# Kernel optimization log

Measured on AMD Instinct MI355X. Metric: run time of the kernel, lower is better.

The kernel has to match this reference:

```python
import jax, jax.numpy as jnp
import numpy as np

N = 50000      # nodes
E = 800000     # edges (avg degree 16)
IN = 128       # in_features
H = 4          # num_heads
OUT = 32       # out_features per head
NEG_SLOPE = 0.2


def setup_inputs() -> dict:
    key = jax.random.key(0)
    k1, k2, k3, k4 = jax.random.split(key, 4)
    h = jax.random.normal(k1, (N, IN), dtype=jnp.float32)
    edge_index = jax.random.randint(k2, (2, E), 0, N, dtype=jnp.int32)
    # xavier-ish init scales
    W = jax.random.normal(k3, (H, IN, OUT), dtype=jnp.float32) * np.float32(np.sqrt(2.0 / (IN + OUT)))
    a = jax.random.normal(k4, (H, 2 * OUT), dtype=jnp.float32) * np.float32(np.sqrt(2.0 / (2 * OUT)))
    return {"h": h, "edge_index": edge_index, "W": W, "a": a}


def reference(h, edge_index, W, a):
    src, dst = edge_index[0], edge_index[1]
    # project per head: [N, H, OUT]
    h_proj = jnp.einsum('ni,hio->nho', h, W)
    # score = leaky_relu(a . [Wh_src || Wh_dst]) ; split a to avoid materializing the concat
    a_src, a_dst = a[:, :OUT], a[:, OUT:]
    s_src = jnp.einsum('nho,ho->nh', h_proj, a_src)   # [N, H]
    s_dst = jnp.einsum('nho,ho->nh', h_proj, a_dst)   # [N, H]
    score = jax.nn.leaky_relu(s_src[src] + s_dst[dst], negative_slope=NEG_SLOPE)  # [E, H]
    # sparse softmax over incoming edges of each dst node
    smax = jax.ops.segment_max(score, dst, num_segments=N)          # [N, H]
    smax = jnp.where(jnp.isfinite(smax), smax, jnp.float32(-1e9))   # nodes with no in-edges
    score_exp = jnp.exp(score - smax[dst])                          # [E, H]
    denom = jax.ops.segment_sum(score_exp, dst, num_segments=N)     # [N, H]
    denom = jnp.maximum(denom, jnp.float32(1e-16))
    alpha = score_exp / denom[dst]                                  # [E, H]
    # weighted aggregation (dropout is identity in eval mode)
    h_src = h_proj[src]                                             # [E, H, OUT]
    h_out = jax.ops.segment_sum(alpha[:, :, None] * h_src, dst, num_segments=N)  # [N, H, OUT]
    h_out = h_out.reshape(N, H * OUT)  # concat=True
    return jax.nn.elu(h_out)
```

## Files before the change

kernel.cpp:

```cpp
#include <hip/hip_runtime.h>

#define NEG_SLOPE 0.2f
#define BCAP 8192

typedef __attribute__((ext_vector_type(8))) short short8;
typedef __attribute__((ext_vector_type(4))) float floatx4;

__device__ __forceinline__ unsigned f2bf(float x) {
  unsigned u = __float_as_uint(x);
  unsigned r = ((u >> 16) & 1u) + 0x7fffu;
  return (u + r) >> 16;
}
__device__ __forceinline__ float bf2f(unsigned hi16) {
  return __uint_as_float(hi16 << 16);
}

__global__ __launch_bounds__(256) void k_gemm(const float* __restrict__ h,
                                              const float* __restrict__ W,
                                              const float* __restrict__ a,
                                              const int* __restrict__ ei,
                                              int* __restrict__ bcur,
                                              uint2* __restrict__ gpairs,
                                              unsigned short* __restrict__ hp16,
                                              float* __restrict__ ssrc,
                                              float* __restrict__ sdst,
                                              int N, int E, int NB1, int NB2) {
  __shared__ unsigned lds_u[16384];
  const int tid = threadIdx.x;

  if (blockIdx.x < NB1) {
    uint2* stage = (uint2*)lds_u;
    int* cnt = (int*)&lds_u[8192];
    int* start = (int*)&lds_u[8448];
    int* cur = (int*)&lds_u[8704];
    int* gbase = (int*)&lds_u[8960];
    int* scn = (int*)&lds_u[9216];
    const int e0 = blockIdx.x * 4096;
    for (int i = tid; i < NB2; i += 256) cnt[i] = 0;
    __syncthreads();
    int sarr[16], darr[16];
#pragma unroll
    for (int j = 0; j < 16; ++j) {
      int e = e0 + j * 256 + tid;
      if (e < E) {
        sarr[j] = ei[e];
        darr[j] = ei[E + e];
        atomicAdd(&cnt[darr[j] >> 8], 1);
      } else {
        darr[j] = -1;
      }
    }
    __syncthreads();
    int s = (tid < NB2) ? cnt[tid] : 0;
    scn[tid] = s;
    __syncthreads();
    for (int off = 1; off < 256; off <<= 1) {
      int t = (tid >= off) ? scn[tid - off] : 0;
      __syncthreads();
      scn[tid] += t;
      __syncthreads();
    }
    if (tid < NB2) {
      start[tid] = scn[tid] - s;
      cur[tid] = scn[tid] - s;
      gbase[tid] = s ? atomicAdd(&bcur[tid], s) : 0;
    }
    __syncthreads();
#pragma unroll
    for (int j = 0; j < 16; ++j) {
      if (darr[j] >= 0) {
        int b = darr[j] >> 8;
        int pos = atomicAdd(&cur[b], 1);
        stage[pos] = make_uint2((unsigned)sarr[j], (unsigned)darr[j]);
      }
    }
    __syncthreads();
    const int total = start[NB2 - 1] + cnt[NB2 - 1];
    for (int u = tid; u < total; u += 256) {
      uint2 pr = stage[u];
      int b = (int)(pr.y >> 8);
      gpairs[(size_t)b * BCAP + gbase[b] + (u - start[b])] = pr;
    }
    __syncthreads();
  }

  const int lane = tid & 63;
  const int wv = tid >> 6;
  const int quad = lane >> 4;
  const int l16 = lane & 15;

#pragma unroll
  for (int it = 0; it < 8; ++it) {
    const int u = it * 256 + tid;
    const int ln = u & 63;
    const int kc = (u >> 6) & 3;
    const int ct = u >> 8;
    const int n = ct * 16 + (ln & 15);
    const int kb = kc * 32 + (ln >> 4) * 8;
    const int head = n >> 5;
    const float* src = W + head * 4096 + (size_t)kb * 32 + (n & 31);
    unsigned hi[4], lo[4];
#pragma unroll
    for (int jj = 0; jj < 4; ++jj) {
      float w0 = src[(2 * jj) * 32];
      float w1 = src[(2 * jj + 1) * 32];
      unsigned h0 = f2bf(w0), h1 = f2bf(w1);
      unsigned l0 = f2bf(w0 - bf2f(h0)), l1 = f2bf(w1 - bf2f(h1));
      hi[jj] = h0 | (h1 << 16);
      lo[jj] = l0 | (l1 << 16);
    }
    *(uint4*)&lds_u[u * 4] = make_uint4(hi[0], hi[1], hi[2], hi[3]);
    *(uint4*)&lds_u[8192 + u * 4] = make_uint4(lo[0], lo[1], lo[2], lo[3]);
  }

  const int row0 = blockIdx.x * 64;
  const int r = row0 + wv * 16 + l16;
  short8 Ah[4], Al[4];
#pragma unroll
  for (int kc = 0; kc < 4; ++kc) {
    float v[8];
    if (r < N) {
      float4 fa = *(const float4*)&h[(size_t)r * 128 + kc * 32 + quad * 8];
      float4 fb = *(const float4*)&h[(size_t)r * 128 + kc * 32 + quad * 8 + 4];
      v[0] = fa.x; v[1] = fa.y; v[2] = fa.z; v[3] = fa.w;
      v[4] = fb.x; v[5] = fb.y; v[6] = fb.z; v[7] = fb.w;
    } else {
#pragma unroll
      for (int j = 0; j < 8; ++j) v[j] = 0.f;
    }
#pragma unroll
    for (int j = 0; j < 8; ++j) {
      unsigned hi = f2bf(v[j]);
      Ah[kc][j] = (short)hi;
      Al[kc][j] = (short)f2bf(v[j] - bf2f(hi));
    }
  }
  __syncthreads();

  floatx4 C[8];
#pragma unroll
  for (int ct = 0; ct < 8; ++ct) {
    floatx4 c = {0.f, 0.f, 0.f, 0.f};
#pragma unroll
    for (int kc = 0; kc < 4; ++kc) {
      int bidx = ((ct * 4 + kc) * 64 + lane) * 4;
      short8 Bh, Bl;
      *(uint4*)&Bh = *(const uint4*)&lds_u[bidx];
      *(uint4*)&Bl = *(const uint4*)&lds_u[8192 + bidx];
      c = __builtin_amdgcn_mfma_f32_16x16x32_bf16(Ah[kc], Bh, c, 0, 0, 0);
      c = __builtin_amdgcn_mfma_f32_16x16x32_bf16(Al[kc], Bh, c, 0, 0, 0);
      c = __builtin_amdgcn_mfma_f32_16x16x32_bf16(Ah[kc], Bl, c, 0, 0, 0);
    }
    C[ct] = c;
  }
  __syncthreads();

  float* epi = (float*)lds_u;
#pragma unroll
  for (int ct = 0; ct < 8; ++ct) {
#pragma unroll
    for (int reg = 0; reg < 4; ++reg) {
      int rr = wv * 16 + quad * 4 + reg;
      epi[rr * 132 + ct * 16 + l16] = C[ct][reg];
    }
  }
  __syncthreads();

  const int row_l = tid >> 2;
  const int hh = tid & 3;
  const int rg = row0 + row_l;
  if (rg < N) {
    const float* rowp = &epi[row_l * 132 + hh * 32];
    float ss = 0.f, sd = 0.f;
    unsigned pka[16];
#pragma unroll
    for (int e = 0; e < 8; ++e) {
      float4 c4 = *(const float4*)&rowp[e * 4];
      float4 as = *(const float4*)&a[hh * 64 + e * 4];
      float4 ad = *(const float4*)&a[hh * 64 + 32 + e * 4];
      ss += c4.x * as.x + c4.y * as.y + c4.z * as.z + c4.w * as.w;
      sd += c4.x * ad.x + c4.y * ad.y + c4.z * ad.z + c4.w * ad.w;
      pka[e * 2] = f2bf(c4.x) | (f2bf(c4.y) << 16);
      pka[e * 2 + 1] = f2bf(c4.z) | (f2bf(c4.w) << 16);
    }
    unsigned short* dst = &hp16[(size_t)rg * 128 + hh * 32];
    *(uint4*)(dst) = make_uint4(pka[0], pka[1], pka[2], pka[3]);
    *(uint4*)(dst + 8) = make_uint4(pka[4], pka[5], pka[6], pka[7]);
    *(uint4*)(dst + 16) = make_uint4(pka[8], pka[9], pka[10], pka[11]);
    *(uint4*)(dst + 24) = make_uint4(pka[12], pka[13], pka[14], pka[15]);
    ssrc[(size_t)rg * 4 + hh] = ss;
    sdst[(size_t)rg * 4 + hh] = sd;
  }
}

__global__ __launch_bounds__(1024) void k_sortagg(const int* __restrict__ bcur,
                                                  const uint2* __restrict__ gpairs,
                                                  const float* __restrict__ ssrc,
                                                  const float* __restrict__ sdst,
                                                  const uint4* __restrict__ hp4,
                                                  float* __restrict__ out, int N) {
  __shared__ int cnt2[128], start2[128], cur2[128], lds[128];
  __shared__ int srcsort[4096];
  __shared__ float sdl[512];
  const int tid = threadIdx.x;
  const int b = blockIdx.x >> 1;
  const int half = blockIdx.x & 1;
  const size_t base = (size_t)b * BCAP;
  const int size = min(bcur[b], BCAP);
  const int d0s = (b << 8) + half * 128;
  const int ndst = min(128, N - d0s);

  if (tid < 128) cnt2[tid] = 0;
  for (int i = tid; i < ndst * 4; i += 1024) sdl[i] = sdst[(size_t)d0s * 4 + i];
  __syncthreads();

  uint2 pr[8];
  int rel[8];
#pragma unroll
  for (int j = 0; j < 8; ++j) {
    const int u = tid + j * 1024;
    if (u < size) pr[j] = gpairs[base + u];
    else pr[j].y = 0xffffffffu;
    rel[j] = (int)pr[j].y - d0s;
    if ((unsigned)rel[j] >= 128u) rel[j] = -1;
  }
#pragma unroll
  for (int j = 0; j < 8; ++j)
    if (rel[j] >= 0) atomicAdd(&cnt2[rel[j]], 1);
  __syncthreads();

  if (tid < 128) lds[tid] = cnt2[tid];
  __syncthreads();
  for (int off = 1; off < 128; off <<= 1) {
    const int t = (tid < 128 && tid >= off) ? lds[tid - off] : 0;
    __syncthreads();
    if (tid < 128) lds[tid] += t;
    __syncthreads();
  }
  if (tid < 128) {
    start2[tid] = lds[tid] - cnt2[tid];
    cur2[tid] = lds[tid] - cnt2[tid];
  }
  __syncthreads();

#pragma unroll
  for (int j = 0; j < 8; ++j) {
    if (rel[j] >= 0) {
      const int pos = atomicAdd(&cur2[rel[j]], 1);
      srcsort[pos] = (int)pr[j].x;
    }
  }
  __syncthreads();

  const int l = tid & 15;
  const int hh = l >> 2;
  for (int dl = tid >> 4; dl < ndst; dl += 64) {
    const int d = d0s + dl;
    const int beg = start2[dl];
    const int end = beg + cnt2[dl];
    const float sdv = sdl[dl * 4 + hh];

    float den[4] = {0.f, 0.f, 0.f, 0.f};
    float acc[8];
#pragma unroll
    for (int j = 0; j < 8; ++j) acc[j] = 0.f;

    int p = beg;
    for (; p + 3 < end; p += 4) {
      int s[4];
      float w[4];
      uint4 v[4];
#pragma unroll
      for (int q = 0; q < 4; ++q) s[q] = srcsort[p + q];
#pragma unroll
      for (int q = 0; q < 4; ++q) {
        float x = ssrc[(size_t)s[q] * 4 + hh] + sdv;
        x = x >= 0.f ? x : NEG_SLOPE * x;
        w[q] = __expf(x);
        v[q] = hp4[(size_t)s[q] * 16 + l];
      }
#pragma unroll
      for (int q = 0; q < 4; ++q) {
        den[q] += w[q];
        acc[0] = fmaf(w[q], bf2f(v[q].x & 0xffffu), acc[0]);
        acc[1] = fmaf(w[q], bf2f(v[q].x >> 16), acc[1]);
        acc[2] = fmaf(w[q], bf2f(v[q].y & 0xffffu), acc[2]);
        acc[3] = fmaf(w[q], bf2f(v[q].y >> 16), acc[3]);
        acc[4] = fmaf(w[q], bf2f(v[q].z & 0xffffu), acc[4]);
        acc[5] = fmaf(w[q], bf2f(v[q].z >> 16), acc[5]);
        acc[6] = fmaf(w[q], bf2f(v[q].w & 0xffffu), acc[6]);
        acc[7] = fmaf(w[q], bf2f(v[q].w >> 16), acc[7]);
      }
    }
    for (; p < end; ++p) {
      const int s0 = srcsort[p];
      float x = ssrc[(size_t)s0 * 4 + hh] + sdv;
      x = x >= 0.f ? x : NEG_SLOPE * x;
      const float w0 = __expf(x);
      const uint4 v0 = hp4[(size_t)s0 * 16 + l];
      den[0] += w0;
      acc[0] = fmaf(w0, bf2f(v0.x & 0xffffu), acc[0]);
      acc[1] = fmaf(w0, bf2f(v0.x >> 16), acc[1]);
      acc[2] = fmaf(w0, bf2f(v0.y & 0xffffu), acc[2]);
      acc[3] = fmaf(w0, bf2f(v0.y >> 16), acc[3]);
      acc[4] = fmaf(w0, bf2f(v0.z & 0xffffu), acc[4]);
      acc[5] = fmaf(w0, bf2f(v0.z >> 16), acc[5]);
      acc[6] = fmaf(w0, bf2f(v0.w & 0xffffu), acc[6]);
      acc[7] = fmaf(w0, bf2f(v0.w >> 16), acc[7]);
    }
    const float rden = 1.f / fmaxf((den[0] + den[1]) + (den[2] + den[3]), 1e-16f);
    float o[8];
#pragma unroll
    for (int j = 0; j < 8; ++j) {
      const float x = acc[j] * rden;
      o[j] = x > 0.f ? x : expm1f(x);
    }
    float* dst = &out[(size_t)d * 128 + l * 8];
    *(float4*)dst = make_float4(o[0], o[1], o[2], o[3]);
    *(float4*)(dst + 4) = make_float4(o[4], o[5], o[6], o[7]);
  }
}

extern "C" void kernel_launch(void* const* d_in, const int* in_sizes, int n_in,
                              void* d_out, int out_size, void* d_ws, size_t ws_size,
                              hipStream_t stream) {
  const float* h = (const float*)d_in[0];
  const int* ei = (const int*)d_in[1];
  const float* W = (const float*)d_in[2];
  const float* a = (const float*)d_in[3];
  float* out = (float*)d_out;
  const int N = in_sizes[0] / 128;
  const int E = in_sizes[1] / 2;
  const int NB2 = (N + 255) >> 8;
  const int NB1 = (E + 4095) / 4096;
  const int NBG = max((N + 63) / 64, NB1);

  char* ws = (char*)d_ws;
  unsigned short* hp16 = (unsigned short*)ws;
  uint2* gpairs = (uint2*)(hp16 + (size_t)N * 128);
  float* ssrc = (float*)(gpairs + (size_t)NB2 * BCAP);
  float* sdst = ssrc + (size_t)N * 4;
  int* bcur = (int*)(sdst + (size_t)N * 4);

  hipMemsetAsync(bcur, 0, NB2 * sizeof(int), stream);
  k_gemm<<<NBG, 256, 0, stream>>>(h, W, a, ei, bcur, gpairs, hp16, ssrc, sdst,
                                  N, E, NB1, NB2);
  k_sortagg<<<NB2 * 2, 1024, 0, stream>>>(bcur, gpairs, ssrc, sdst,
                                          (const uint4*)hp16, out, N);
}
```

Before: 142.0 us.

## Pack edge pairs into 32-bit words, swizzle block order, widen gather loop

Each bucketed edge is now stored as one 32-bit word, with the source index in the low 24 bits and the destination's offset within its bucket in the high 8 bits. This halves the scratch traffic for the edge list between the two kernels. The aggregation kernel remaps block IDs so consecutive blocks land on different XCD chunks, and it sets a launch-bounds occupancy hint. Its gather loop now handles 6 edges per iteration with masked tail loads instead of a 4-wide loop plus a scalar remainder. The packing assumes node indices fit in 24 bits, and the masked tail issues redundant loads for padding slots.

```diff
diff --git a/kernel.cpp b/kernel.cpp
--- a/kernel.cpp
+++ b/kernel.cpp
@@ -20,7 +20,7 @@
                                               const float* __restrict__ a,
                                               const int* __restrict__ ei,
                                               int* __restrict__ bcur,
-                                              uint2* __restrict__ gpairs,
+                                              unsigned* __restrict__ gpairs,
                                               unsigned short* __restrict__ hp16,
                                               float* __restrict__ ssrc,
                                               float* __restrict__ sdst,
@@ -79,7 +79,8 @@
     for (int u = tid; u < total; u += 256) {
       uint2 pr = stage[u];
       int b = (int)(pr.y >> 8);
-      gpairs[(size_t)b * BCAP + gbase[b] + (u - start[b])] = pr;
+      gpairs[(size_t)b * BCAP + gbase[b] + (u - start[b])] =
+          pr.x | ((pr.y & 255u) << 24);
     }
     __syncthreads();
   }
@@ -193,18 +194,21 @@
   }
 }
 
-__global__ __launch_bounds__(1024) void k_sortagg(const int* __restrict__ bcur,
-                                                  const uint2* __restrict__ gpairs,
-                                                  const float* __restrict__ ssrc,
-                                                  const float* __restrict__ sdst,
-                                                  const uint4* __restrict__ hp4,
-                                                  float* __restrict__ out, int N) {
+__global__ __launch_bounds__(1024, 8) void k_sortagg(const int* __restrict__ bcur,
+                                                     const unsigned* __restrict__ gpairs,
+                                                     const float* __restrict__ ssrc,
+                                                     const float* __restrict__ sdst,
+                                                     const uint4* __restrict__ hp4,
+                                                     float* __restrict__ out, int N) {
   __shared__ int cnt2[128], start2[128], cur2[128], lds[128];
   __shared__ int srcsort[4096];
   __shared__ float sdl[512];
   const int tid = threadIdx.x;
-  const int b = blockIdx.x >> 1;
-  const int half = blockIdx.x & 1;
+  const int u0 = blockIdx.x;
+  const int chunk = gridDim.x >> 3;
+  const int id = ((gridDim.x & 7) == 0) ? (u0 & 7) * chunk + (u0 >> 3) : u0;
+  const int b = id >> 1;
+  const int half = id & 1;
   const size_t base = (size_t)b * BCAP;
   const int size = min(bcur[b], BCAP);
   const int d0s = (b << 8) + half * 128;
@@ -214,15 +218,14 @@
   for (int i = tid; i < ndst * 4; i += 1024) sdl[i] = sdst[(size_t)d0s * 4 + i];
   __syncthreads();
 
-  uint2 pr[8];
+  unsigned pr[8];
   int rel[8];
 #pragma unroll
   for (int j = 0; j < 8; ++j) {
     const int u = tid + j * 1024;
-    if (u < size) pr[j] = gpairs[base + u];
-    else pr[j].y = 0xffffffffu;
-    rel[j] = (int)pr[j].y - d0s;
-    if ((unsigned)rel[j] >= 128u) rel[j] = -1;
+    pr[j] = (u < size) ? gpairs[base + u] : 0xffffffffu;
+    rel[j] = (int)(pr[j] >> 24) - half * 128;
+    if (pr[j] == 0xffffffffu || (unsigned)rel[j] >= 128u) rel[j] = -1;
   }
 #pragma unroll
   for (int j = 0; j < 8; ++j)
@@ -247,7 +250,7 @@
   for (int j = 0; j < 8; ++j) {
     if (rel[j] >= 0) {
       const int pos = atomicAdd(&cur2[rel[j]], 1);
-      srcsort[pos] = (int)pr[j].x;
+      srcsort[pos] = (int)(pr[j] & 0x00ffffffu);
     }
   }
   __syncthreads();
@@ -265,23 +268,25 @@
 #pragma unroll
     for (int j = 0; j < 8; ++j) acc[j] = 0.f;
 
-    int p = beg;
-    for (; p + 3 < end; p += 4) {
-      int s[4];
-      float w[4];
-      uint4 v[4];
-#pragma unroll
-      for (int q = 0; q < 4; ++q) s[q] = srcsort[p + q];
-#pragma unroll
-      for (int q = 0; q < 4; ++q) {
+    for (int p = beg; p < end; p += 6) {
+      int s[6];
+      float w[6];
+      uint4 v[6];
+#pragma unroll
+      for (int q = 0; q < 6; ++q) {
+        const int pp = p + q;
+        s[q] = srcsort[pp < end ? pp : beg];
+      }
+#pragma unroll
+      for (int q = 0; q < 6; ++q) {
         float x = ssrc[(size_t)s[q] * 4 + hh] + sdv;
         x = x >= 0.f ? x : NEG_SLOPE * x;
-        w[q] = __expf(x);
+        w[q] = (p + q < end) ? __expf(x) : 0.f;
         v[q] = hp4[(size_t)s[q] * 16 + l];
       }
 #pragma unroll
-      for (int q = 0; q < 4; ++q) {
-        den[q] += w[q];
+      for (int q = 0; q < 6; ++q) {
+        den[q & 3] += w[q];
         acc[0] = fmaf(w[q], bf2f(v[q].x & 0xffffu), acc[0]);
         acc[1] = fmaf(w[q], bf2f(v[q].x >> 16), acc[1]);
         acc[2] = fmaf(w[q], bf2f(v[q].y & 0xffffu), acc[2]);
@@ -291,22 +296,6 @@
         acc[6] = fmaf(w[q], bf2f(v[q].w & 0xffffu), acc[6]);
         acc[7] = fmaf(w[q], bf2f(v[q].w >> 16), acc[7]);
       }
-    }
-    for (; p < end; ++p) {
-      const int s0 = srcsort[p];
-      float x = ssrc[(size_t)s0 * 4 + hh] + sdv;
-      x = x >= 0.f ? x : NEG_SLOPE * x;
-      const float w0 = __expf(x);
-      const uint4 v0 = hp4[(size_t)s0 * 16 + l];
-      den[0] += w0;
-      acc[0] = fmaf(w0, bf2f(v0.x & 0xffffu), acc[0]);
-      acc[1] = fmaf(w0, bf2f(v0.x >> 16), acc[1]);
-      acc[2] = fmaf(w0, bf2f(v0.y & 0xffffu), acc[2]);
-      acc[3] = fmaf(w0, bf2f(v0.y >> 16), acc[3]);
-      acc[4] = fmaf(w0, bf2f(v0.z & 0xffffu), acc[4]);
-      acc[5] = fmaf(w0, bf2f(v0.z >> 16), acc[5]);
-      acc[6] = fmaf(w0, bf2f(v0.w & 0xffffu), acc[6]);
-      acc[7] = fmaf(w0, bf2f(v0.w >> 16), acc[7]);
     }
     const float rden = 1.f / fmaxf((den[0] + den[1]) + (den[2] + den[3]), 1e-16f);
     float o[8];
@@ -337,7 +326,7 @@
 
   char* ws = (char*)d_ws;
   unsigned short* hp16 = (unsigned short*)ws;
-  uint2* gpairs = (uint2*)(hp16 + (size_t)N * 128);
+  unsigned* gpairs = (unsigned*)(hp16 + (size_t)N * 128);
   float* ssrc = (float*)(gpairs + (size_t)NB2 * BCAP);
   float* sdst = ssrc + (size_t)N * 4;
   int* bcur = (int*)(sdst + (size_t)N * 4);
```

Result: slower. 180.9 us (+27.4%).
